# Optimization experiments

Hardware: AMD Instinct MI355X
Metric: run time of the kernel (lower is better)

The kernel has to match this reference:

```python
import jax, jax.numpy as jnp
import numpy as np

D_MODEL, D_STATE, D_CONV = 1024, 16, 4
B, L = 2, 2048


def setup_inputs() -> dict:
    key = jax.random.key(0)
    ks = jax.random.split(key, 12)
    d, n, k = D_MODEL, D_STATE, D_CONV
    s = lambda fan_in: 1.0 / np.sqrt(fan_in)
    inp = {
        "x": jax.random.normal(ks[0], (B, L, d), dtype=jnp.float32),
        # Linear weights stored as (in, out): y = x @ W + b
        "W_in": jax.random.uniform(ks[1], (d, 2 * d), minval=-s(d), maxval=s(d)),
        "b_in": jax.random.uniform(ks[2], (2 * d,), minval=-s(d), maxval=s(d)),
        # depthwise conv: (out_ch=d, in_ch/groups=1, kernel=k)
        "W_conv": jax.random.uniform(ks[3], (d, 1, k), minval=-s(k), maxval=s(k)),
        "b_conv": jax.random.uniform(ks[4], (d,), minval=-s(k), maxval=s(k)),
        "W_xp": jax.random.uniform(ks[5], (d, 3 * n), minval=-s(d), maxval=s(d)),
        "b_xp": jax.random.uniform(ks[6], (3 * n,), minval=-s(d), maxval=s(d)),
        "W_dt": jax.random.uniform(ks[7], (n, d), minval=-s(n), maxval=s(n)),
        "b_dt": jax.random.uniform(ks[8], (d,), minval=-s(n), maxval=s(n)),
        # A param initialized as in torch: arange(1, n+1) tiled over d rows
        "A_log": jnp.tile(jnp.arange(1, n + 1, dtype=jnp.float32), (d, 1)),
        "W_out": jax.random.uniform(ks[9], (d, d), minval=-s(d), maxval=s(d)),
        "b_out": jax.random.uniform(ks[10], (d,), minval=-s(d), maxval=s(d)),
    }
    return inp


def _forward(x, W_in, b_in, W_conv, b_conv, W_xp, b_xp, W_dt, b_dt, A_log, W_out, b_out):
    n = D_STATE
    k = W_conv.shape[-1]
    silu = jax.nn.silu

    xz = x @ W_in + b_in                       # (B, L, 2d)
    u, z = jnp.split(xz, 2, axis=-1)

    # causal depthwise conv1d: torch pads k-1 both sides then keeps first L
    uc = jnp.transpose(u, (0, 2, 1))           # (B, d, L)
    uc = jax.lax.conv_general_dilated(
        uc, W_conv, window_strides=(1,), padding=[(k - 1, 0)],
        dimension_numbers=("NCH", "OIH", "NCH"), feature_group_count=D_MODEL,
    ) + b_conv[None, :, None]
    u = silu(jnp.transpose(uc, (0, 2, 1)))     # (B, L, d)

    x_db = u @ W_xp + b_xp                     # (B, L, 3n)
    dt_in, Bm, Cm = jnp.split(x_db, [n, 2 * n], axis=-1)
    dt = jax.nn.softplus(dt_in @ W_dt + b_dt)  # (B, L, d)

    A = -jnp.exp(A_log)                        # (d, n)
    dA = jnp.exp(jnp.einsum("bld,dn->bldn", dt, A))          # (B, L, d, n)
    dBu = (dt * u)[..., None] * Bm[:, :, None, :]              # (B, L, d, n)

    def step(h, inputs):
        dA_t, dBu_t, C_t = inputs              # (B,d,n), (B,d,n), (B,n)
        h = dA_t * h + dBu_t
        y = jnp.einsum("bdn,bn->bd", h, C_t)
        return h, y

    h0 = jnp.zeros((x.shape[0], D_MODEL, n), dtype=x.dtype)
    xs = (jnp.transpose(dA, (1, 0, 2, 3)),
          jnp.transpose(dBu, (1, 0, 2, 3)),
          jnp.transpose(Cm, (1, 0, 2)))
    _, ys = jax.lax.scan(step, h0, xs)         # (L, B, d)
    y = jnp.transpose(ys, (1, 0, 2))           # (B, L, d)

    y = y * silu(z)
    return y @ W_out + b_out


def reference(x, W_in, b_in, W_conv, b_conv, W_xp, b_xp, W_dt, b_dt, A_log, W_out, b_out):
    return _forward(x, W_in, b_in, W_conv, b_conv, W_xp, b_xp, W_dt, b_dt, A_log, W_out, b_out)
```

## Files before the change

kernel.cpp:

```cpp
#include <hip/hip_runtime.h>
#include <math.h>

#define D_MODEL 1024
#define D_STATE 16
#define BATCH   2
#define SEQ     2048
#define M_ROWS  (BATCH*SEQ)
#define KP      3072
#define CH      32
#define NCHUNK  (SEQ/CH)

typedef unsigned short ushortT;
typedef ushortT ushortx4 __attribute__((ext_vector_type(4)));
typedef ushortT ushortx8 __attribute__((ext_vector_type(8)));
typedef short   shortx8  __attribute__((ext_vector_type(8)));
typedef float   f32x4    __attribute__((ext_vector_type(4)));

__device__ __forceinline__ float silu_f(float x) {
    return x / (1.0f + __expf(-x));
}
__device__ __forceinline__ ushortT f2bf_rne(float f) {
    unsigned u = __float_as_uint(f);
    u += 0x7FFF + ((u >> 16) & 1);
    return (ushortT)(u >> 16);
}
__device__ __forceinline__ float bf2f(ushortT h) {
    return __uint_as_float(((unsigned)h) << 16);
}

__global__ __launch_bounds__(256)
void split_x_kernel(const float* __restrict__ X, ushortT* __restrict__ Xs)
{
    int gid = blockIdx.x * 256 + threadIdx.x;
    const int KQ = D_MODEL / 4;
    if (gid >= M_ROWS * KQ) return;
    int row = gid / KQ, kc = gid % KQ;
    float4 v = *reinterpret_cast<const float4*>(X + (size_t)row * D_MODEL + kc * 4);
    float vv[4] = {v.x, v.y, v.z, v.w};
    ushortx4 h, l;
#pragma unroll
    for (int i = 0; i < 4; ++i) {
        ushortT hi = f2bf_rne(vv[i]);
        h[i] = hi;
        l[i] = f2bf_rne(vv[i] - bf2f(hi));
    }
    ushortT* base = Xs + (size_t)row * KP + kc * 4;
    *(ushortx4*)(base)              = h;
    *(ushortx4*)(base + D_MODEL)     = l;
    *(ushortx4*)(base + 2 * D_MODEL) = h;
}

__global__ __launch_bounds__(256)
void gate_split_kernel(const float* __restrict__ Y, const float* __restrict__ Z,
                       ushortT* __restrict__ Ys)
{
    int gid = blockIdx.x * 256 + threadIdx.x;
    const int KQ = D_MODEL / 4;
    if (gid >= M_ROWS * KQ) return;
    int row = gid / KQ, kc = gid % KQ;
    float4 vy = *reinterpret_cast<const float4*>(Y + (size_t)row * D_MODEL + kc * 4);
    float4 vz = *reinterpret_cast<const float4*>(Z + (size_t)row * D_MODEL + kc * 4);
    float vv[4] = {vy.x * silu_f(vz.x), vy.y * silu_f(vz.y),
                   vy.z * silu_f(vz.z), vy.w * silu_f(vz.w)};
    ushortx4 h, l;
#pragma unroll
    for (int i = 0; i < 4; ++i) {
        ushortT hi = f2bf_rne(vv[i]);
        h[i] = hi;
        l[i] = f2bf_rne(vv[i] - bf2f(hi));
    }
    ushortT* base = Ys + (size_t)row * KP + kc * 4;
    *(ushortx4*)(base)              = h;
    *(ushortx4*)(base + D_MODEL)     = l;
    *(ushortx4*)(base + 2 * D_MODEL) = h;
}

__global__ __launch_bounds__(256)
void wsplit_t_kernel(const float* __restrict__ W, ushortT* __restrict__ Wt, int N)
{
    __shared__ float tile[32][33];
    const int K = D_MODEL;
    int nb = blockIdx.x * 32, kb = blockIdx.y * 32;
    int tx = threadIdx.x & 31;
    int ty = threadIdx.x >> 5;
#pragma unroll
    for (int i = 0; i < 4; ++i) {
        int k = ty + i * 8;
        tile[k][tx] = W[(size_t)(kb + k) * N + nb + tx];
    }
    __syncthreads();
#pragma unroll
    for (int i = 0; i < 4; ++i) {
        int n = ty + i * 8;
        float v = tile[tx][n];
        ushortT hi = f2bf_rne(v);
        ushortT lo = f2bf_rne(v - bf2f(hi));
        ushortT* base = Wt + (size_t)(nb + n) * KP + kb + tx;
        base[0]     = hi;
        base[K]     = hi;
        base[2 * K] = lo;
    }
}

__global__ __launch_bounds__(256)
void wsplit_xp_kernel(const float* __restrict__ W, ushortT* __restrict__ Wt)
{
    int gid = blockIdx.x * 256 + threadIdx.x;
    if (gid >= 64 * D_MODEL) return;
    int k = gid & (D_MODEL - 1);
    int n = gid >> 10;
    ushortT hi = 0, lo = 0;
    if (n < 48) {
        float v = W[(size_t)k * 48 + n];
        hi = f2bf_rne(v);
        lo = f2bf_rne(v - bf2f(hi));
    }
    ushortT* base = Wt + (size_t)n * KP + k;
    base[0]           = hi;
    base[D_MODEL]     = hi;
    base[2 * D_MODEL] = lo;
}

__global__ __launch_bounds__(256)
void gemm_mfma_split(const ushortT* __restrict__ A,
                     const ushortT* __restrict__ Bt,
                     const float* __restrict__ bias,
                     float* __restrict__ C0,
                     float* __restrict__ C1,
                     int N, int split)
{
    __shared__ char lds[32768];
    char* Asm = lds;
    char* Bsm = lds + 16384;

    const int tid  = threadIdx.x;
    const int lane = tid & 63;
    const int wid  = tid >> 6;
    const int wr   = wid >> 1;
    const int wc   = wid & 1;
    const int brow = blockIdx.y * 128;
    const int bcol = blockIdx.x * 128;

    f32x4 acc[4][4];
#pragma unroll
    for (int i = 0; i < 4; ++i)
#pragma unroll
        for (int j = 0; j < 4; ++j) {
            acc[i][j][0] = 0.f; acc[i][j][1] = 0.f;
            acc[i][j][2] = 0.f; acc[i][j][3] = 0.f;
        }

    const ushortT* Ag = A  + (size_t)brow * KP;
    const ushortT* Bg = Bt + (size_t)bcol * KP;

    ushortx8 ra0[4], rb0[4], ra1[4], rb1[4];

#define SLOAD(ra, rb, k0)                                                      \
    {                                                                          \
        _Pragma("unroll")                                                      \
        for (int q = 0; q < 4; ++q) {                                          \
            int slot = tid + q * 256;                                          \
            int row = slot >> 3, kc = slot & 7;                                \
            ra[q] = *(const ushortx8*)(Ag + (size_t)row * KP + (k0) + kc * 8); \
            rb[q] = *(const ushortx8*)(Bg + (size_t)row * KP + (k0) + kc * 8); \
        }                                                                      \
    }

#define SWRITE(ra, rb)                                                         \
    {                                                                          \
        _Pragma("unroll")                                                      \
        for (int q = 0; q < 4; ++q) {                                          \
            int slot = tid + q * 256;                                          \
            int row = slot >> 3, kc = slot & 7;                                \
            int byt = row * 128 + ((kc * 16) ^ ((row & 7) << 4));              \
            *(ushortx8*)(Asm + byt) = ra[q];                                   \
            *(ushortx8*)(Bsm + byt) = rb[q];                                   \
        }                                                                      \
    }

#define COMPUTE()                                                              \
    {                                                                          \
        _Pragma("unroll")                                                      \
        for (int ks = 0; ks < 2; ++ks) {                                       \
            shortx8 af[4], bfr[4];                                             \
            _Pragma("unroll")                                                  \
            for (int mt = 0; mt < 4; ++mt) {                                   \
                int row = wr * 64 + mt * 16 + (lane & 15);                     \
                int kc = ks * 4 + (lane >> 4);                                 \
                int byt = row * 128 + ((kc * 16) ^ ((row & 7) << 4));          \
                af[mt] = *(const shortx8*)(Asm + byt);                         \
            }                                                                  \
            _Pragma("unroll")                                                  \
            for (int nt = 0; nt < 4; ++nt) {                                   \
                int row = wc * 64 + nt * 16 + (lane & 15);                     \
                int kc = ks * 4 + (lane >> 4);                                 \
                int byt = row * 128 + ((kc * 16) ^ ((row & 7) << 4));          \
                bfr[nt] = *(const shortx8*)(Bsm + byt);                        \
            }                                                                  \
            _Pragma("unroll")                                                  \
            for (int mt = 0; mt < 4; ++mt)                                     \
                _Pragma("unroll")                                              \
                for (int nt = 0; nt < 4; ++nt)                                 \
                    acc[mt][nt] = __builtin_amdgcn_mfma_f32_16x16x32_bf16(     \
                        af[mt], bfr[nt], acc[mt][nt], 0, 0, 0);                \
        }                                                                      \
    }

    SLOAD(ra0, rb0, 0);
    const int NS = KP / 64;
    for (int s = 0; s < NS; s += 2) {
        __syncthreads();
        SWRITE(ra0, rb0);
        __syncthreads();
        if (s + 1 < NS) SLOAD(ra1, rb1, (s + 1) * 64);
        COMPUTE();
        __syncthreads();
        SWRITE(ra1, rb1);
        __syncthreads();
        if (s + 2 < NS) SLOAD(ra0, rb0, (s + 2) * 64);
        COMPUTE();
    }

#undef SLOAD
#undef SWRITE
#undef COMPUTE

    const bool inC0  = (bcol < split);
    float* dst       = inC0 ? C0 : C1;
    const int ldc    = inC0 ? split : (N - split);
    const int cb     = bcol - (inC0 ? 0 : split);

#pragma unroll
    for (int mt = 0; mt < 4; ++mt)
#pragma unroll
        for (int nt = 0; nt < 4; ++nt)
#pragma unroll
            for (int j = 0; j < 4; ++j) {
                int r  = brow + wr * 64 + mt * 16 + (lane >> 4) * 4 + j;
                int cg = wc * 64 + nt * 16 + (lane & 15);
                dst[(size_t)r * ldc + cb + cg] = acc[mt][nt][j] + bias[bcol + cg];
            }
}

__global__ __launch_bounds__(256)
void gemm_xp_mfma(const ushortT* __restrict__ A,
                  const ushortT* __restrict__ Bt,
                  float* __restrict__ Part)
{
    __shared__ char lds[24576];
    char* Asm = lds;
    char* Bsm = lds + 16384;

    const int tid  = threadIdx.x;
    const int lane = tid & 63;
    const int wid  = tid >> 6;
    const int ksp  = blockIdx.x;
    const int brow = blockIdx.y * 128;
    const int kbase = ksp * (KP / 4);

    f32x4 acc[2][4];
#pragma unroll
    for (int i = 0; i < 2; ++i)
#pragma unroll
        for (int j = 0; j < 4; ++j) {
            acc[i][j][0] = 0.f; acc[i][j][1] = 0.f;
            acc[i][j][2] = 0.f; acc[i][j][3] = 0.f;
        }

    const ushortT* Ag = A  + (size_t)brow * KP + kbase;
    const ushortT* Bg = Bt + kbase;

    for (int s = 0; s < 12; ++s) {
        const int k0 = s * 64;
        ushortx8 ra[4], rb[2];
#pragma unroll
        for (int q = 0; q < 4; ++q) {
            int slot = tid + q * 256;
            int row = slot >> 3, kc = slot & 7;
            ra[q] = *(const ushortx8*)(Ag + (size_t)row * KP + k0 + kc * 8);
        }
#pragma unroll
        for (int q = 0; q < 2; ++q) {
            int slot = tid + q * 256;
            int row = slot >> 3, kc = slot & 7;
            rb[q] = *(const ushortx8*)(Bg + (size_t)row * KP + k0 + kc * 8);
        }
        __syncthreads();
#pragma unroll
        for (int q = 0; q < 4; ++q) {
            int slot = tid + q * 256;
            int row = slot >> 3, kc = slot & 7;
            int byt = row * 128 + ((kc * 16) ^ ((row & 7) << 4));
            *(ushortx8*)(Asm + byt) = ra[q];
        }
#pragma unroll
        for (int q = 0; q < 2; ++q) {
            int slot = tid + q * 256;
            int row = slot >> 3, kc = slot & 7;
            int byt = row * 128 + ((kc * 16) ^ ((row & 7) << 4));
            *(ushortx8*)(Bsm + byt) = rb[q];
        }
        __syncthreads();
#pragma unroll
        for (int ks = 0; ks < 2; ++ks) {
            shortx8 af[2], bfr[4];
#pragma unroll
            for (int mt = 0; mt < 2; ++mt) {
                int row = wid * 32 + mt * 16 + (lane & 15);
                int kc = ks * 4 + (lane >> 4);
                int byt = row * 128 + ((kc * 16) ^ ((row & 7) << 4));
                af[mt] = *(const shortx8*)(Asm + byt);
            }
#pragma unroll
            for (int nt = 0; nt < 4; ++nt) {
                int row = nt * 16 + (lane & 15);
                int kc = ks * 4 + (lane >> 4);
                int byt = row * 128 + ((kc * 16) ^ ((row & 7) << 4));
                bfr[nt] = *(const shortx8*)(Bsm + byt);
            }
#pragma unroll
            for (int mt = 0; mt < 2; ++mt)
#pragma unroll
                for (int nt = 0; nt < 4; ++nt)
                    acc[mt][nt] = __builtin_amdgcn_mfma_f32_16x16x32_bf16(
                        af[mt], bfr[nt], acc[mt][nt], 0, 0, 0);
        }
        __syncthreads();
    }

    float* dst = Part + (size_t)ksp * M_ROWS * 64;
#pragma unroll
    for (int mt = 0; mt < 2; ++mt)
#pragma unroll
        for (int nt = 0; nt < 4; ++nt)
#pragma unroll
            for (int j = 0; j < 4; ++j) {
                int r  = brow + wid * 32 + mt * 16 + (lane >> 4) * 4 + j;
                int cg = nt * 16 + (lane & 15);
                dst[(size_t)r * 64 + cg] = acc[mt][nt][j];
            }
}

__global__ __launch_bounds__(256)
void xp_combine_kernel(const float* __restrict__ Part,
                       const float* __restrict__ b_xp,
                       float* __restrict__ x_db)
{
    int gid = blockIdx.x * 256 + threadIdx.x;
    if (gid >= M_ROWS * 12) return;
    int row = gid / 12, q = gid % 12;
    float4 a = *reinterpret_cast<const float4*>(b_xp + q * 4);
#pragma unroll
    for (int s = 0; s < 4; ++s) {
        float4 p = *reinterpret_cast<const float4*>(
            Part + ((size_t)s * M_ROWS + row) * 64 + q * 4);
        a.x += p.x; a.y += p.y; a.z += p.z; a.w += p.w;
    }
    *reinterpret_cast<float4*>(x_db + (size_t)row * 48 + q * 4) = a;
}

__global__ __launch_bounds__(256)
void conv_silu_split_kernel(const float* __restrict__ u_raw,
                            const float* __restrict__ W_conv,
                            const float* __restrict__ b_conv,
                            float* __restrict__ u_out,
                            ushortT* __restrict__ Us)
{
    int gid = blockIdx.x * 256 + threadIdx.x;
    if (gid >= M_ROWS * D_MODEL) return;
    int c = gid % D_MODEL;
    int t = (gid / D_MODEL) % SEQ;
    int b = gid / (D_MODEL * SEQ);

    float w0 = W_conv[c * 4 + 0], w1 = W_conv[c * 4 + 1];
    float w2 = W_conv[c * 4 + 2], w3 = W_conv[c * 4 + 3];
    const float* base = u_raw + (size_t)b * SEQ * D_MODEL + c;

    float acc = b_conv[c];
    if (t >= 3) acc = fmaf(base[(size_t)(t - 3) * D_MODEL], w0, acc);
    if (t >= 2) acc = fmaf(base[(size_t)(t - 2) * D_MODEL], w1, acc);
    if (t >= 1) acc = fmaf(base[(size_t)(t - 1) * D_MODEL], w2, acc);
    acc = fmaf(base[(size_t)t * D_MODEL], w3, acc);

    float v = silu_f(acc);
    u_out[gid] = v;

    ushortT hi = f2bf_rne(v);
    ushortT lo = f2bf_rne(v - bf2f(hi));
    size_t row = (size_t)(gid / D_MODEL);
    ushortT* ub = Us + row * KP + c;
    ub[0]           = hi;
    ub[D_MODEL]     = lo;
    ub[2 * D_MODEL] = hi;
}

__global__ __launch_bounds__(256)
void dt_kernel(const float* __restrict__ x_db,
               const float* __restrict__ W_dt,
               const float* __restrict__ b_dt,
               float* __restrict__ dt)
{
    int gid = blockIdx.x * 256 + threadIdx.x;
    if (gid >= M_ROWS * D_MODEL) return;
    int row = gid / D_MODEL, c = gid % D_MODEL;
    const float* din = x_db + (size_t)row * 48;
    float acc = b_dt[c];
#pragma unroll
    for (int i = 0; i < 16; ++i)
        acc = fmaf(din[i], W_dt[i * D_MODEL + c], acc);
    float sp = fmaxf(acc, 0.0f) + log1pf(expf(-fabsf(acc)));
    dt[gid] = sp;
}

__global__ __launch_bounds__(256)
void scan_chunk_local(const float* __restrict__ dt,
                      const float* __restrict__ u,
                      const float* __restrict__ x_db,
                      const float* __restrict__ A_log,
                      float* __restrict__ Pbuf,
                      float* __restrict__ Hloc)
{
    int gid = blockIdx.x * 256 + threadIdx.x;
    if (gid >= BATCH * NCHUNK * D_MODEL) return;
    int c     = gid % D_MODEL;
    int rem   = gid / D_MODEL;
    int chunk = rem % NCHUNK;
    int b     = rem / NCHUNK;

    float a[16], h[16];
#pragma unroll
    for (int i = 0; i < 16; ++i) {
        a[i] = -__expf(A_log[c * 16 + i]);
        h[i] = 0.f;
    }

    float dtsum = 0.f;
    size_t row = (size_t)b * SEQ + (size_t)chunk * CH;
    for (int t = 0; t < CH; ++t, ++row) {
        float dtv = dt[row * D_MODEL + c];
        float uv  = u[row * D_MODEL + c];
        const float* xb = x_db + row * 48;
        float du = dtv * uv;
        dtsum += dtv;
#pragma unroll
        for (int i = 0; i < 16; ++i) {
            float dA = __expf(dtv * a[i]);
            h[i] = fmaf(dA, h[i], du * xb[16 + i]);
        }
    }

    size_t obase = ((size_t)(b * NCHUNK + chunk) * 16) * D_MODEL + c;
#pragma unroll
    for (int i = 0; i < 16; ++i) {
        Pbuf[obase + (size_t)i * D_MODEL] = __expf(a[i] * dtsum);
        Hloc[obase + (size_t)i * D_MODEL] = h[i];
    }
}

__global__ __launch_bounds__(256)
void scan_combine(const float* __restrict__ Pbuf,
                  const float* __restrict__ Hloc,
                  float* __restrict__ Hin)
{
    int gid = blockIdx.x * 256 + threadIdx.x;
    if (gid >= BATCH * 16 * D_MODEL) return;
    int c   = gid % D_MODEL;
    int rem = gid / D_MODEL;
    int i   = rem % 16;
    int b   = rem / 16;

    const size_t stride = (size_t)16 * D_MODEL;
    size_t idx = ((size_t)(b * NCHUNK) * 16 + i) * D_MODEL + c;

    float h  = 0.f;
    float Pn = Pbuf[idx];
    float Hn = Hloc[idx];
    for (int ch = 0; ch < NCHUNK; ++ch) {
        float Pc = Pn, Hc = Hn;
        if (ch + 1 < NCHUNK) {
            Pn = Pbuf[idx + stride];
            Hn = Hloc[idx + stride];
        }
        Hin[idx] = h;
        h = fmaf(Pc, h, Hc);
        idx += stride;
    }
}

__global__ __launch_bounds__(256)
void scan_chunk_final(const float* __restrict__ dt,
                      const float* __restrict__ u,
                      const float* __restrict__ x_db,
                      const float* __restrict__ A_log,
                      const float* __restrict__ Hin,
                      float* __restrict__ y)
{
    int gid = blockIdx.x * 256 + threadIdx.x;
    if (gid >= BATCH * NCHUNK * D_MODEL) return;
    int c     = gid % D_MODEL;
    int rem   = gid / D_MODEL;
    int chunk = rem % NCHUNK;
    int b     = rem / NCHUNK;

    size_t ibase = ((size_t)(b * NCHUNK + chunk) * 16) * D_MODEL + c;

    float a[16], h[16];
#pragma unroll
    for (int i = 0; i < 16; ++i) {
        a[i] = -__expf(A_log[c * 16 + i]);
        h[i] = Hin[ibase + (size_t)i * D_MODEL];
    }

    size_t row = (size_t)b * SEQ + (size_t)chunk * CH;
    for (int t = 0; t < CH; ++t, ++row) {
        float dtv = dt[row * D_MODEL + c];
        float uv  = u[row * D_MODEL + c];
        const float* xb = x_db + row * 48;
        float du = dtv * uv;
        float yv = 0.f;
#pragma unroll
        for (int i = 0; i < 16; ++i) {
            float dA = __expf(dtv * a[i]);
            h[i] = fmaf(dA, h[i], du * xb[16 + i]);
            yv   = fmaf(h[i], xb[32 + i], yv);
        }
        y[row * D_MODEL + c] = yv;
    }
}

extern "C" void kernel_launch(void* const* d_in, const int* in_sizes, int n_in,
                              void* d_out, int out_size, void* d_ws, size_t ws_size,
                              hipStream_t stream)
{
    const float* x      = (const float*)d_in[0];
    const float* W_in   = (const float*)d_in[1];
    const float* b_in   = (const float*)d_in[2];
    const float* W_conv = (const float*)d_in[3];
    const float* b_conv = (const float*)d_in[4];
    const float* W_xp   = (const float*)d_in[5];
    const float* b_xp   = (const float*)d_in[6];
    const float* W_dt   = (const float*)d_in[7];
    const float* b_dt   = (const float*)d_in[8];
    const float* A_log  = (const float*)d_in[9];
    const float* W_out  = (const float*)d_in[10];
    const float* b_out  = (const float*)d_in[11];
    float* out = (float*)d_out;

    float* ws = (float*)d_ws;
    const size_t S  = (size_t)M_ROWS * D_MODEL;
    const size_t SC = (size_t)BATCH * NCHUNK * 16 * D_MODEL;
    float* u_raw  = ws;
    float* z      = ws + S;
    float* u_conv = ws + 2 * S;
    float* dtbuf  = ws + 3 * S;
    float* x_db   = ws + 4 * S;
    float* Pbuf   = ws + 4 * S + 196608;
    float* HlocB  = Pbuf + SC;
    float* HinB   = HlocB + SC;
    ushortT* xs   = (ushortT*)(HinB + SC);
    ushortT* wt   = xs + (size_t)M_ROWS * KP;
    ushortT* wxp  = wt + (size_t)2048 * KP;
    float*   part = (float*)(wxp + (size_t)64 * KP);

    dim3 blk(256);

    wsplit_t_kernel<<<dim3(2 * D_MODEL / 32, D_MODEL / 32), blk, 0, stream>>>(W_in, wt, 2 * D_MODEL);
    split_x_kernel<<<dim3(M_ROWS * (D_MODEL / 4) / 256), blk, 0, stream>>>(x, xs);

    gemm_mfma_split<<<dim3(2 * D_MODEL / 128, M_ROWS / 128), blk, 0, stream>>>(
        xs, wt, b_in, u_raw, z, 2 * D_MODEL, D_MODEL);

    conv_silu_split_kernel<<<dim3(M_ROWS * D_MODEL / 256), blk, 0, stream>>>(
        u_raw, W_conv, b_conv, u_conv, xs);

    wsplit_xp_kernel<<<dim3(64 * D_MODEL / 256), blk, 0, stream>>>(W_xp, wxp);
    gemm_xp_mfma<<<dim3(4, M_ROWS / 128), blk, 0, stream>>>(xs, wxp, part);
    xp_combine_kernel<<<dim3(M_ROWS * 12 / 256), blk, 0, stream>>>(part, b_xp, x_db);

    dt_kernel<<<dim3(M_ROWS * D_MODEL / 256), blk, 0, stream>>>(x_db, W_dt, b_dt, dtbuf);

    scan_chunk_local<<<dim3(BATCH * NCHUNK * D_MODEL / 256), blk, 0, stream>>>(
        dtbuf, u_conv, x_db, A_log, Pbuf, HlocB);
    scan_combine<<<dim3(BATCH * 16 * D_MODEL / 256), blk, 0, stream>>>(Pbuf, HlocB, HinB);
    scan_chunk_final<<<dim3(BATCH * NCHUNK * D_MODEL / 256), blk, 0, stream>>>(
        dtbuf, u_conv, x_db, A_log, HinB, u_raw);

    wsplit_t_kernel<<<dim3(D_MODEL / 32, D_MODEL / 32), blk, 0, stream>>>(W_out, wt, D_MODEL);
    gate_split_kernel<<<dim3(M_ROWS * (D_MODEL / 4) / 256), blk, 0, stream>>>(u_raw, z, xs);

    gemm_mfma_split<<<dim3(D_MODEL / 128, M_ROWS / 128), blk, 0, stream>>>(
        xs, wt, b_out, out, out, D_MODEL, D_MODEL);
}
```

Measured before the change: 259.0 us.

## Fuse dt projection and gating into scan kernels, swizzle GEMM workgroups

Removes the separate dt kernel and computes the dt projection plus softplus inside both scan passes. The scan passes now rebuild u from the bf16 hi/lo split buffer, so the fp32 u_conv buffer is no longer written. The final scan pass applies the silu(z) gate and writes the bf16-split operand for the output GEMM directly, which removes the gate kernel and the fp32 y round trip. The GEMM also gets an XCD-style workgroup index swizzle. The trade-offs are that dt is now computed twice, u carries only about 16 bits of mantissa, and the final scan reads and writes the same split buffer through __restrict__ pointers.

```diff
diff --git a/kernel.cpp b/kernel.cpp
--- a/kernel.cpp
+++ b/kernel.cpp
@@ -45,31 +45,6 @@
         l[i] = f2bf_rne(vv[i] - bf2f(hi));
     }
     ushortT* base = Xs + (size_t)row * KP + kc * 4;
-    *(ushortx4*)(base)              = h;
-    *(ushortx4*)(base + D_MODEL)     = l;
-    *(ushortx4*)(base + 2 * D_MODEL) = h;
-}
-
-__global__ __launch_bounds__(256)
-void gate_split_kernel(const float* __restrict__ Y, const float* __restrict__ Z,
-                       ushortT* __restrict__ Ys)
-{
-    int gid = blockIdx.x * 256 + threadIdx.x;
-    const int KQ = D_MODEL / 4;
-    if (gid >= M_ROWS * KQ) return;
-    int row = gid / KQ, kc = gid % KQ;
-    float4 vy = *reinterpret_cast<const float4*>(Y + (size_t)row * D_MODEL + kc * 4);
-    float4 vz = *reinterpret_cast<const float4*>(Z + (size_t)row * D_MODEL + kc * 4);
-    float vv[4] = {vy.x * silu_f(vz.x), vy.y * silu_f(vz.y),
-                   vy.z * silu_f(vz.z), vy.w * silu_f(vz.w)};
-    ushortx4 h, l;
-#pragma unroll
-    for (int i = 0; i < 4; ++i) {
-        ushortT hi = f2bf_rne(vv[i]);
-        h[i] = hi;
-        l[i] = f2bf_rne(vv[i] - bf2f(hi));
-    }
-    ushortT* base = Ys + (size_t)row * KP + kc * 4;
     *(ushortx4*)(base)              = h;
     *(ushortx4*)(base + D_MODEL)     = l;
     *(ushortx4*)(base + 2 * D_MODEL) = h;
@@ -138,8 +113,15 @@
     const int wid  = tid >> 6;
     const int wr   = wid >> 1;
     const int wc   = wid & 1;
-    const int brow = blockIdx.y * 128;
-    const int bcol = blockIdx.x * 128;
+
+    const int nwg  = gridDim.x * gridDim.y;
+    const int wgid = blockIdx.y * gridDim.x + blockIdx.x;
+    const int qc   = nwg >> 3;
+    const int swz  = (wgid & 7) * qc + (wgid >> 3);
+    const int bx   = swz % gridDim.x;
+    const int by   = swz / gridDim.x;
+    const int brow = by * 128;
+    const int bcol = bx * 128;
 
     f32x4 acc[4][4];
 #pragma unroll
@@ -363,7 +345,6 @@
 void conv_silu_split_kernel(const float* __restrict__ u_raw,
                             const float* __restrict__ W_conv,
                             const float* __restrict__ b_conv,
-                            float* __restrict__ u_out,
                             ushortT* __restrict__ Us)
 {
     int gid = blockIdx.x * 256 + threadIdx.x;
@@ -383,7 +364,6 @@
     acc = fmaf(base[(size_t)t * D_MODEL], w3, acc);
 
     float v = silu_f(acc);
-    u_out[gid] = v;
 
     ushortT hi = f2bf_rne(v);
     ushortT lo = f2bf_rne(v - bf2f(hi));
@@ -395,28 +375,11 @@
 }
 
 __global__ __launch_bounds__(256)
-void dt_kernel(const float* __restrict__ x_db,
-               const float* __restrict__ W_dt,
-               const float* __restrict__ b_dt,
-               float* __restrict__ dt)
-{
-    int gid = blockIdx.x * 256 + threadIdx.x;
-    if (gid >= M_ROWS * D_MODEL) return;
-    int row = gid / D_MODEL, c = gid % D_MODEL;
-    const float* din = x_db + (size_t)row * 48;
-    float acc = b_dt[c];
-#pragma unroll
-    for (int i = 0; i < 16; ++i)
-        acc = fmaf(din[i], W_dt[i * D_MODEL + c], acc);
-    float sp = fmaxf(acc, 0.0f) + log1pf(expf(-fabsf(acc)));
-    dt[gid] = sp;
-}
-
-__global__ __launch_bounds__(256)
-void scan_chunk_local(const float* __restrict__ dt,
-                      const float* __restrict__ u,
+void scan_chunk_local(const ushortT* __restrict__ Us,
                       const float* __restrict__ x_db,
                       const float* __restrict__ A_log,
+                      const float* __restrict__ W_dt,
+                      const float* __restrict__ b_dt,
                       float* __restrict__ Pbuf,
                       float* __restrict__ Hloc)
 {
@@ -427,19 +390,26 @@
     int chunk = rem % NCHUNK;
     int b     = rem / NCHUNK;
 
-    float a[16], h[16];
+    float a[16], h[16], wdt[16];
 #pragma unroll
     for (int i = 0; i < 16; ++i) {
-        a[i] = -__expf(A_log[c * 16 + i]);
-        h[i] = 0.f;
-    }
+        a[i]   = -__expf(A_log[c * 16 + i]);
+        h[i]   = 0.f;
+        wdt[i] = W_dt[i * D_MODEL + c];
+    }
+    const float bdt = b_dt[c];
 
     float dtsum = 0.f;
     size_t row = (size_t)b * SEQ + (size_t)chunk * CH;
     for (int t = 0; t < CH; ++t, ++row) {
-        float dtv = dt[row * D_MODEL + c];
-        float uv  = u[row * D_MODEL + c];
         const float* xb = x_db + row * 48;
+        float acc = bdt;
+#pragma unroll
+        for (int i = 0; i < 16; ++i)
+            acc = fmaf(xb[i], wdt[i], acc);
+        float dtv = fmaxf(acc, 0.0f) + log1pf(expf(-fabsf(acc)));
+
+        float uv = bf2f(Us[row * KP + c]) + bf2f(Us[row * KP + D_MODEL + c]);
         float du = dtv * uv;
         dtsum += dtv;
 #pragma unroll
@@ -488,12 +458,14 @@
 }
 
 __global__ __launch_bounds__(256)
-void scan_chunk_final(const float* __restrict__ dt,
-                      const float* __restrict__ u,
+void scan_chunk_final(const ushortT* __restrict__ Us,
                       const float* __restrict__ x_db,
                       const float* __restrict__ A_log,
+                      const float* __restrict__ W_dt,
+                      const float* __restrict__ b_dt,
                       const float* __restrict__ Hin,
-                      float* __restrict__ y)
+                      const float* __restrict__ z,
+                      ushortT* __restrict__ Ys)
 {
     int gid = blockIdx.x * 256 + threadIdx.x;
     if (gid >= BATCH * NCHUNK * D_MODEL) return;
@@ -504,18 +476,25 @@
 
     size_t ibase = ((size_t)(b * NCHUNK + chunk) * 16) * D_MODEL + c;
 
-    float a[16], h[16];
+    float a[16], h[16], wdt[16];
 #pragma unroll
     for (int i = 0; i < 16; ++i) {
-        a[i] = -__expf(A_log[c * 16 + i]);
-        h[i] = Hin[ibase + (size_t)i * D_MODEL];
-    }
+        a[i]   = -__expf(A_log[c * 16 + i]);
+        h[i]   = Hin[ibase + (size_t)i * D_MODEL];
+        wdt[i] = W_dt[i * D_MODEL + c];
+    }
+    const float bdt = b_dt[c];
 
     size_t row = (size_t)b * SEQ + (size_t)chunk * CH;
     for (int t = 0; t < CH; ++t, ++row) {
-        float dtv = dt[row * D_MODEL + c];
-        float uv  = u[row * D_MODEL + c];
         const float* xb = x_db + row * 48;
+        float acc = bdt;
+#pragma unroll
+        for (int i = 0; i < 16; ++i)
+            acc = fmaf(xb[i], wdt[i], acc);
+        float dtv = fmaxf(acc, 0.0f) + log1pf(expf(-fabsf(acc)));
+
+        float uv = bf2f(Us[row * KP + c]) + bf2f(Us[row * KP + D_MODEL + c]);
         float du = dtv * uv;
         float yv = 0.f;
 #pragma unroll
@@ -524,7 +503,14 @@
             h[i] = fmaf(dA, h[i], du * xb[16 + i]);
             yv   = fmaf(h[i], xb[32 + i], yv);
         }
-        y[row * D_MODEL + c] = yv;
+
+        float g = yv * silu_f(z[row * D_MODEL + c]);
+        ushortT hi = f2bf_rne(g);
+        ushortT lo = f2bf_rne(g - bf2f(hi));
+        ushortT* yb = Ys + row * KP + c;
+        yb[0]           = hi;
+        yb[D_MODEL]     = lo;
+        yb[2 * D_MODEL] = hi;
     }
 }
 
@@ -551,8 +537,6 @@
     const size_t SC = (size_t)BATCH * NCHUNK * 16 * D_MODEL;
     float* u_raw  = ws;
     float* z      = ws + S;
-    float* u_conv = ws + 2 * S;
-    float* dtbuf  = ws + 3 * S;
     float* x_db   = ws + 4 * S;
     float* Pbuf   = ws + 4 * S + 196608;
     float* HlocB  = Pbuf + SC;
@@ -571,22 +555,20 @@
         xs, wt, b_in, u_raw, z, 2 * D_MODEL, D_MODEL);
 
     conv_silu_split_kernel<<<dim3(M_ROWS * D_MODEL / 256), blk, 0, stream>>>(
-        u_raw, W_conv, b_conv, u_conv, xs);
+        u_raw, W_conv, b_conv, xs);
 
     wsplit_xp_kernel<<<dim3(64 * D_MODEL / 256), blk, 0, stream>>>(W_xp, wxp);
     gemm_xp_mfma<<<dim3(4, M_ROWS / 128), blk, 0, stream>>>(xs, wxp, part);
     xp_combine_kernel<<<dim3(M_ROWS * 12 / 256), blk, 0, stream>>>(part, b_xp, x_db);
 
-    dt_kernel<<<dim3(M_ROWS * D_MODEL / 256), blk, 0, stream>>>(x_db, W_dt, b_dt, dtbuf);
-
     scan_chunk_local<<<dim3(BATCH * NCHUNK * D_MODEL / 256), blk, 0, stream>>>(
-        dtbuf, u_conv, x_db, A_log, Pbuf, HlocB);
+        xs, x_db, A_log, W_dt, b_dt, Pbuf, HlocB);
     scan_combine<<<dim3(BATCH * 16 * D_MODEL / 256), blk, 0, stream>>>(Pbuf, HlocB, HinB);
+
+    wsplit_t_kernel<<<dim3(D_MODEL / 32, D_MODEL / 32), blk, 0, stream>>>(W_out, wt, D_MODEL);
+
     scan_chunk_final<<<dim3(BATCH * NCHUNK * D_MODEL / 256), blk, 0, stream>>>(
-        dtbuf, u_conv, x_db, A_log, HinB, u_raw);
-
-    wsplit_t_kernel<<<dim3(D_MODEL / 32, D_MODEL / 32), blk, 0, stream>>>(W_out, wt, D_MODEL);
-    gate_split_kernel<<<dim3(M_ROWS * (D_MODEL / 4) / 256), blk, 0, stream>>>(u_raw, z, xs);
+        xs, x_db, A_log, W_dt, b_dt, HinB, z, xs);
 
     gemm_mfma_split<<<dim3(D_MODEL / 128, M_ROWS / 128), blk, 0, stream>>>(
         xs, wt, b_out, out, out, D_MODEL, D_MODEL);
```

New measurement: 253.4 us. -2.2%, faster.
